# Performance work log

Measured on AMD Instinct MI355X. Metric: run time of the kernel, lower is better.

Reference implementation:

```python
import jax, jax.numpy as jnp
import numpy as np


def _lstm_cell(x, h, c, Wih, Whh, b):
    # PyTorch LSTMCell gate order: i, f, g, o; b = b_ih + b_hh
    z = x @ Wih.T + h @ Whh.T + b
    i, f, g, o = jnp.split(z, 4, axis=-1)
    c_new = jax.nn.sigmoid(f) * c + jax.nn.sigmoid(i) * jnp.tanh(g)
    h_new = jax.nn.sigmoid(o) * jnp.tanh(c_new)
    return h_new, c_new


B, T, F, H, HOR, OUT = 16384, 96, 16, 64, 24, 16


def setup_inputs() -> dict:
    key = jax.random.key(0)
    ks = jax.random.split(key, 20)
    s = 1.0 / np.sqrt(H)

    def u(k, shape):
        return jax.random.uniform(k, shape, jnp.float32, -s, s)

    return {
        "X": jax.random.normal(ks[0], (B, T, F), jnp.float32),
        "bias": jax.random.normal(ks[1], (B, 1, OUT), jnp.float32),
        "X_mask": jnp.ones((B, T), dtype=bool),
        # encoder layer 0 (in=F) and layer 1 (in=H)
        "enc_Wih0": u(ks[2], (4 * H, F)), "enc_Whh0": u(ks[3], (4 * H, H)), "enc_b0": u(ks[4], (4 * H,)),
        "enc_Wih1": u(ks[5], (4 * H, H)), "enc_Whh1": u(ks[6], (4 * H, H)), "enc_b1": u(ks[7], (4 * H,)),
        # decoder layers (in=H)
        "dec_Wih0": u(ks[8], (4 * H, H)), "dec_Whh0": u(ks[9], (4 * H, H)), "dec_b0": u(ks[10], (4 * H,)),
        "dec_Wih1": u(ks[11], (4 * H, H)), "dec_Whh1": u(ks[12], (4 * H, H)), "dec_b1": u(ks[13], (4 * H,)),
        "reg_W1": u(ks[14], (H, H)), "reg_b1": u(ks[15], (H,)),
        "reg_W2": u(ks[16], (OUT, H)), "reg_b2": u(ks[17], (OUT,)),
    }


def reference(X, bias, X_mask,
              enc_Wih0, enc_Whh0, enc_b0, enc_Wih1, enc_Whh1, enc_b1,
              dec_Wih0, dec_Whh0, dec_b0, dec_Wih1, dec_Whh1, dec_b1,
              reg_W1, reg_b1, reg_W2, reg_b2):
    b = X.shape[0]
    z = jnp.zeros((b, H), X.dtype)

    # ---- encoder: scan over time, 2 stacked LSTMCells ----
    def enc_step(carry, x_t):
        h0, c0, h1, c1 = carry
        h0, c0 = _lstm_cell(x_t, h0, c0, enc_Wih0, enc_Whh0, enc_b0)
        h1, c1 = _lstm_cell(h0, h1, c1, enc_Wih1, enc_Whh1, enc_b1)
        return (h0, c0, h1, c1), None

    (h0, _, h1, _), _ = jax.lax.scan(enc_step, (z, z, z, z),
                                     jnp.swapaxes(X, 0, 1))  # [T,B,F]

    # ---- decoder: fresh c (zeros), h from encoder, h_t starts at top-layer h ----
    last_bias = bias[:, -1]  # [B, OUT]

    def dec_step(carry, _):
        h_t, dh0, dc0, dh1, dc1 = carry
        h_t, dc0 = _lstm_cell(h_t, dh0, dc0, dec_Wih0, dec_Whh0, dec_b0)
        dh0 = h_t
        h_t, dc1 = _lstm_cell(h_t, dh1, dc1, dec_Wih1, dec_Whh1, dec_b1)
        dh1 = h_t
        y = jax.nn.relu(h_t @ reg_W1.T + reg_b1) @ reg_W2.T + reg_b2
        y = y + last_bias  # add_last_step_val=True
        return (h_t, dh0, dc0, dh1, dc1), y

    _, ys = jax.lax.scan(dec_step, (h1, h0, z, h1, z), None, length=HOR)
    return jnp.swapaxes(ys, 0, 1)  # [B, horizon, OUT]
```

## Files before the change

kernel.cpp:

```cpp
#include <hip/hip_runtime.h>

typedef short v8s __attribute__((ext_vector_type(8)));
typedef float v4f __attribute__((ext_vector_type(4)));

__device__ __forceinline__ unsigned cvtpk(float lo, float hi) {
    unsigned r;
    asm("v_cvt_pk_bf16_f32 %0, %1, %2" : "=v"(r) : "v"(lo), "v"(hi));
    return r;
}
__device__ __forceinline__ v8s pack8(float4 f0, float4 f1) {
    union { unsigned u[4]; v8s v; } r;
    r.u[0] = cvtpk(f0.x, f0.y); r.u[1] = cvtpk(f0.z, f0.w);
    r.u[2] = cvtpk(f1.x, f1.y); r.u[3] = cvtpk(f1.z, f1.w);
    return r.v;
}
__device__ __forceinline__ float sigm(float x) {
    float e = __builtin_amdgcn_exp2f(-1.44269504f * x);
    return __builtin_amdgcn_rcpf(1.0f + e);
}
__device__ __forceinline__ float tanh_(float x) {
    float e = __builtin_amdgcn_exp2f(2.88539008f * x);
    return 1.0f - 2.0f * __builtin_amdgcn_rcpf(1.0f + e);
}
__device__ __forceinline__ v4f mfma(v8s a, v8s b, v4f c) {
    return __builtin_amdgcn_mfma_f32_16x16x32_bf16(a, b, c, 0, 0, 0);
}
__device__ __forceinline__ v8s ldwf(const float* W, int rowElems, int n, int k0) {
    const float* p = W + (size_t)n * rowElems + k0;
    union { unsigned u[4]; v8s v; } r;
    #pragma unroll
    for (int j = 0; j < 4; ++j) r.u[j] = cvtpk(p[2 * j], p[2 * j + 1]);
    return r.v;
}

__global__ __launch_bounds__(256, 2) void seq2seq(
    const float* __restrict__ X,
    const float* __restrict__ bias,
    const float* __restrict__ eWih0, const float* __restrict__ eWhh0, const float* __restrict__ eb0,
    const float* __restrict__ eWih1, const float* __restrict__ eWhh1, const float* __restrict__ eb1,
    const float* __restrict__ dWih0, const float* __restrict__ dWhh0, const float* __restrict__ db0,
    const float* __restrict__ dWih1, const float* __restrict__ dWhh1, const float* __restrict__ db1,
    const float* __restrict__ rW1, const float* __restrict__ rb1,
    const float* __restrict__ rW2, const float* __restrict__ rb2,
    float* __restrict__ out)
{
    __shared__ __align__(16) short sh0[2][2048];
    __shared__ __align__(16) short sh1[2][2048];
    __shared__ __align__(16) short sy1[2048];

    const int tid  = threadIdx.x;
    const int lane = tid & 63;
    const int w    = tid >> 6;
    const int lo   = lane & 15, hi = lane >> 4;
    const int wg   = blockIdx.x;

    for (int i = tid; i < 1024; i += 256) {
        ((int*)sh0)[1024 + i] = 0;
        ((int*)sh1)[1024 + i] = 0;
    }

    const int wsidx = (w >> 1) * 512 + (((2 * w) + (lo >> 3)) & 3) * 128 + hi * 32 + (lo & 7);

    v8s wf[4][4][2];
    float bz0[4], bz1[4];
    #pragma unroll
    for (int g = 0; g < 4; ++g) {
        const int n = (w + 4 * g) * 16 + lo;
        v8s z = {0, 0, 0, 0, 0, 0, 0, 0};
        wf[0][g][0] = (hi < 2) ? ldwf(eWih0, 16, n, (hi & 1) * 8) : z;
        wf[0][g][1] = z;
        #pragma unroll
        for (int kk = 0; kk < 2; ++kk) {
            wf[1][g][kk] = ldwf(eWhh0, 64, n, kk * 32 + hi * 8);
            wf[2][g][kk] = ldwf(eWih1, 64, n, kk * 32 + hi * 8);
            wf[3][g][kk] = ldwf(eWhh1, 64, n, kk * 32 + hi * 8);
        }
        bz0[g] = eb0[g * 64 + w * 16 + lo];
        bz1[g] = eb1[g * 64 + w * 16 + lo];
    }

    float c0[2][4] = {{0.f,0.f,0.f,0.f},{0.f,0.f,0.f,0.f}};
    float c1[2][4] = {{0.f,0.f,0.f,0.f},{0.f,0.f,0.f,0.f}};
    __syncthreads();

    const float* xb = X + (size_t)(wg * 32 + lo) * 1536 + (hi & 1) * 8;

    for (int t = 0; t < 96; ++t) {
        const int pw = t & 1, pr = pw ^ 1;
        v4f acc[4][2];
        #pragma unroll
        for (int g = 0; g < 4; ++g)
            #pragma unroll
            for (int mt = 0; mt < 2; ++mt)
                acc[g][mt] = (v4f){bz0[g], bz0[g], bz0[g], bz0[g]};
        #pragma unroll
        for (int mt = 0; mt < 2; ++mt) {
            const float* p = xb + (size_t)mt * 16 * 1536 + t * 16;
            const v8s ax = pack8(*(const float4*)p, *(const float4*)(p + 4));
            #pragma unroll
            for (int g = 0; g < 4; ++g) acc[g][mt] = mfma(ax, wf[0][g][0], acc[g][mt]);
        }
        #pragma unroll
        for (int kk = 0; kk < 2; ++kk)
            #pragma unroll
            for (int mt = 0; mt < 2; ++mt) {
                const v8s ah = *(const v8s*)&sh0[pr][(mt * 2 + kk) * 512 + lane * 8];
                #pragma unroll
                for (int g = 0; g < 4; ++g) acc[g][mt] = mfma(ah, wf[1][g][kk], acc[g][mt]);
            }
        #pragma unroll
        for (int mt = 0; mt < 2; ++mt) {
            float hh[4];
            #pragma unroll
            for (int q = 0; q < 4; ++q) {
                float cc = sigm(acc[1][mt][q]) * c0[mt][q] + sigm(acc[0][mt][q]) * tanh_(acc[2][mt][q]);
                c0[mt][q] = cc;
                hh[q] = sigm(acc[3][mt][q]) * tanh_(cc);
            }
            #pragma unroll
            for (int qp = 0; qp < 2; ++qp) {
                unsigned pk = cvtpk(hh[2 * qp], hh[2 * qp + 1]);
                short* b = &sh0[pw][wsidx + mt * 1024 + qp * 16];
                b[0] = (short)pk; b[8] = (short)(pk >> 16);
            }
        }
        __syncthreads();
        #pragma unroll
        for (int g = 0; g < 4; ++g)
            #pragma unroll
            for (int mt = 0; mt < 2; ++mt)
                acc[g][mt] = (v4f){bz1[g], bz1[g], bz1[g], bz1[g]};
        #pragma unroll
        for (int kk = 0; kk < 2; ++kk)
            #pragma unroll
            for (int mt = 0; mt < 2; ++mt) {
                const v8s ah = *(const v8s*)&sh0[pw][(mt * 2 + kk) * 512 + lane * 8];
                const v8s bh = *(const v8s*)&sh1[pr][(mt * 2 + kk) * 512 + lane * 8];
                #pragma unroll
                for (int g = 0; g < 4; ++g) {
                    acc[g][mt] = mfma(ah, wf[2][g][kk], acc[g][mt]);
                    acc[g][mt] = mfma(bh, wf[3][g][kk], acc[g][mt]);
                }
            }
        #pragma unroll
        for (int mt = 0; mt < 2; ++mt) {
            float hh[4];
            #pragma unroll
            for (int q = 0; q < 4; ++q) {
                float cc = sigm(acc[1][mt][q]) * c1[mt][q] + sigm(acc[0][mt][q]) * tanh_(acc[2][mt][q]);
                c1[mt][q] = cc;
                hh[q] = sigm(acc[3][mt][q]) * tanh_(cc);
            }
            #pragma unroll
            for (int qp = 0; qp < 2; ++qp) {
                unsigned pk = cvtpk(hh[2 * qp], hh[2 * qp + 1]);
                short* b = &sh1[pw][wsidx + mt * 1024 + qp * 16];
                b[0] = (short)pk; b[8] = (short)(pk >> 16);
            }
        }
    }
    __syncthreads();

    #pragma unroll
    for (int g = 0; g < 4; ++g) {
        const int n = (w + 4 * g) * 16 + lo;
        #pragma unroll
        for (int kk = 0; kk < 2; ++kk) {
            wf[0][g][kk] = ldwf(dWih0, 64, n, kk * 32 + hi * 8);
            wf[1][g][kk] = ldwf(dWhh0, 64, n, kk * 32 + hi * 8);
            wf[2][g][kk] = ldwf(dWih1, 64, n, kk * 32 + hi * 8);
            wf[3][g][kk] = ldwf(dWhh1, 64, n, kk * 32 + hi * 8);
        }
        bz0[g] = db0[g * 64 + w * 16 + lo];
        bz1[g] = db1[g * 64 + w * 16 + lo];
    }
    v8s w1f[2], w2f[2];
    #pragma unroll
    for (int kk = 0; kk < 2; ++kk) {
        w1f[kk] = ldwf(rW1, 64, w * 16 + lo, kk * 32 + hi * 8);
        w2f[kk] = ldwf(rW2, 64, lo, kk * 32 + hi * 8);
    }
    const float hb1 = rb1[w * 16 + lo];
    const float hb2 = rb2[lo];
    float lb[2][4];
    #pragma unroll
    for (int mt = 0; mt < 2; ++mt)
        #pragma unroll
        for (int q = 0; q < 4; ++q) {
            lb[mt][q] = bias[(size_t)(wg * 32 + mt * 16 + hi * 4 + q) * 16 + lo];
            c0[mt][q] = 0.f;
            c1[mt][q] = 0.f;
        }

    for (int s = 0; s < 24; ++s) {
        const int pw = s & 1, pr = pw ^ 1;
        v4f acc[4][2];
        #pragma unroll
        for (int g = 0; g < 4; ++g)
            #pragma unroll
            for (int mt = 0; mt < 2; ++mt)
                acc[g][mt] = (v4f){bz0[g], bz0[g], bz0[g], bz0[g]};
        #pragma unroll
        for (int kk = 0; kk < 2; ++kk)
            #pragma unroll
            for (int mt = 0; mt < 2; ++mt) {
                const v8s ah = *(const v8s*)&sh1[pr][(mt * 2 + kk) * 512 + lane * 8];
                const v8s bh = *(const v8s*)&sh0[pr][(mt * 2 + kk) * 512 + lane * 8];
                #pragma unroll
                for (int g = 0; g < 4; ++g) {
                    acc[g][mt] = mfma(ah, wf[0][g][kk], acc[g][mt]);
                    acc[g][mt] = mfma(bh, wf[1][g][kk], acc[g][mt]);
                }
            }
        #pragma unroll
        for (int mt = 0; mt < 2; ++mt) {
            float hh[4];
            #pragma unroll
            for (int q = 0; q < 4; ++q) {
                float cc = sigm(acc[1][mt][q]) * c0[mt][q] + sigm(acc[0][mt][q]) * tanh_(acc[2][mt][q]);
                c0[mt][q] = cc;
                hh[q] = sigm(acc[3][mt][q]) * tanh_(cc);
            }
            #pragma unroll
            for (int qp = 0; qp < 2; ++qp) {
                unsigned pk = cvtpk(hh[2 * qp], hh[2 * qp + 1]);
                short* b = &sh0[pw][wsidx + mt * 1024 + qp * 16];
                b[0] = (short)pk; b[8] = (short)(pk >> 16);
            }
        }
        __syncthreads();
        if (w == 0 && s > 0) {
            v4f a2[2];
            #pragma unroll
            for (int mt = 0; mt < 2; ++mt) a2[mt] = (v4f){hb2, hb2, hb2, hb2};
            #pragma unroll
            for (int kk = 0; kk < 2; ++kk)
                #pragma unroll
                for (int mt = 0; mt < 2; ++mt) {
                    const v8s a = *(const v8s*)&sy1[(mt * 2 + kk) * 512 + lane * 8];
                    a2[mt] = mfma(a, w2f[kk], a2[mt]);
                }
            #pragma unroll
            for (int mt = 0; mt < 2; ++mt)
                #pragma unroll
                for (int q = 0; q < 4; ++q) {
                    size_t row = (size_t)(wg * 32 + mt * 16 + hi * 4 + q);
                    out[row * 384 + (s - 1) * 16 + lo] = a2[mt][q] + lb[mt][q];
                }
        }
        #pragma unroll
        for (int g = 0; g < 4; ++g)
            #pragma unroll
            for (int mt = 0; mt < 2; ++mt)
                acc[g][mt] = (v4f){bz1[g], bz1[g], bz1[g], bz1[g]};
        #pragma unroll
        for (int kk = 0; kk < 2; ++kk)
            #pragma unroll
            for (int mt = 0; mt < 2; ++mt) {
                const v8s ah = *(const v8s*)&sh0[pw][(mt * 2 + kk) * 512 + lane * 8];
                const v8s bh = *(const v8s*)&sh1[pr][(mt * 2 + kk) * 512 + lane * 8];
                #pragma unroll
                for (int g = 0; g < 4; ++g) {
                    acc[g][mt] = mfma(ah, wf[2][g][kk], acc[g][mt]);
                    acc[g][mt] = mfma(bh, wf[3][g][kk], acc[g][mt]);
                }
            }
        #pragma unroll
        for (int mt = 0; mt < 2; ++mt) {
            float hh[4];
            #pragma unroll
            for (int q = 0; q < 4; ++q) {
                float cc = sigm(acc[1][mt][q]) * c1[mt][q] + sigm(acc[0][mt][q]) * tanh_(acc[2][mt][q]);
                c1[mt][q] = cc;
                hh[q] = sigm(acc[3][mt][q]) * tanh_(cc);
            }
            #pragma unroll
            for (int qp = 0; qp < 2; ++qp) {
                unsigned pk = cvtpk(hh[2 * qp], hh[2 * qp + 1]);
                short* b = &sh1[pw][wsidx + mt * 1024 + qp * 16];
                b[0] = (short)pk; b[8] = (short)(pk >> 16);
            }
        }
        __syncthreads();
        v4f ay[2];
        #pragma unroll
        for (int mt = 0; mt < 2; ++mt) ay[mt] = (v4f){hb1, hb1, hb1, hb1};
        #pragma unroll
        for (int kk = 0; kk < 2; ++kk)
            #pragma unroll
            for (int mt = 0; mt < 2; ++mt) {
                const v8s ah = *(const v8s*)&sh1[pw][(mt * 2 + kk) * 512 + lane * 8];
                ay[mt] = mfma(ah, w1f[kk], ay[mt]);
            }
        #pragma unroll
        for (int mt = 0; mt < 2; ++mt) {
            #pragma unroll
            for (int qp = 0; qp < 2; ++qp) {
                unsigned pk = cvtpk(fmaxf(ay[mt][2 * qp], 0.f), fmaxf(ay[mt][2 * qp + 1], 0.f));
                short* b = &sy1[wsidx + mt * 1024 + qp * 16];
                b[0] = (short)pk; b[8] = (short)(pk >> 16);
            }
        }
    }
    __syncthreads();
    if (w == 0) {
        v4f a2[2];
        #pragma unroll
        for (int mt = 0; mt < 2; ++mt) a2[mt] = (v4f){hb2, hb2, hb2, hb2};
        #pragma unroll
        for (int kk = 0; kk < 2; ++kk)
            #pragma unroll
            for (int mt = 0; mt < 2; ++mt) {
                const v8s a = *(const v8s*)&sy1[(mt * 2 + kk) * 512 + lane * 8];
                a2[mt] = mfma(a, w2f[kk], a2[mt]);
            }
        #pragma unroll
        for (int mt = 0; mt < 2; ++mt)
            #pragma unroll
            for (int q = 0; q < 4; ++q) {
                size_t row = (size_t)(wg * 32 + mt * 16 + hi * 4 + q);
                out[row * 384 + 23 * 16 + lo] = a2[mt][q] + lb[mt][q];
            }
    }
}

extern "C" void kernel_launch(void* const* d_in, const int* in_sizes, int n_in,
                              void* d_out, int out_size, void* d_ws, size_t ws_size,
                              hipStream_t stream) {
    seq2seq<<<dim3(512), dim3(256), 0, stream>>>(
        (const float*)d_in[0],
        (const float*)d_in[1],
        (const float*)d_in[3],  (const float*)d_in[4],  (const float*)d_in[5],
        (const float*)d_in[6],  (const float*)d_in[7],  (const float*)d_in[8],
        (const float*)d_in[9],  (const float*)d_in[10], (const float*)d_in[11],
        (const float*)d_in[12], (const float*)d_in[13], (const float*)d_in[14],
        (const float*)d_in[15], (const float*)d_in[16],
        (const float*)d_in[17], (const float*)d_in[18],
        (float*)d_out);
}
```

Before: 590.5 us.

## Fuse LSTM gate nonlinearities into one cell function with fewer reciprocals; prefetch X loads

Replaces the separate sigmoid/tanh calls with an algebraically combined cell update. It uses five exp2 and two rcp per element instead of five exp2 and five rcp, which cuts transcendental-unit pressure on the recurrent critical path. It also hoists the X global loads to the top of each encoder step, reorders the recurrent MFMAs ahead of the input MFMAs so load latency is hidden, and unrolls both time loops by two. The combined formula clamps the exponent of c but not the gate exponents, so overflow to inf for large pre-activations could produce NaN. Unrolling may also raise register pressure under launch_bounds(256,2).

```diff
diff --git a/kernel.cpp b/kernel.cpp
--- a/kernel.cpp
+++ b/kernel.cpp
@@ -14,14 +14,6 @@
     r.u[2] = cvtpk(f1.x, f1.y); r.u[3] = cvtpk(f1.z, f1.w);
     return r.v;
 }
-__device__ __forceinline__ float sigm(float x) {
-    float e = __builtin_amdgcn_exp2f(-1.44269504f * x);
-    return __builtin_amdgcn_rcpf(1.0f + e);
-}
-__device__ __forceinline__ float tanh_(float x) {
-    float e = __builtin_amdgcn_exp2f(2.88539008f * x);
-    return 1.0f - 2.0f * __builtin_amdgcn_rcpf(1.0f + e);
-}
 __device__ __forceinline__ v4f mfma(v8s a, v8s b, v4f c) {
     return __builtin_amdgcn_mfma_f32_16x16x32_bf16(a, b, c, 0, 0, 0);
 }
@@ -31,6 +23,20 @@
     #pragma unroll
     for (int j = 0; j < 4; ++j) r.u[j] = cvtpk(p[2 * j], p[2 * j + 1]);
     return r.v;
+}
+
+__device__ __forceinline__ float cell(float zi, float zf, float zg, float zo, float& c) {
+    const float NL = -1.44269504f, PG = 2.88539008f;
+    float ei = __builtin_amdgcn_exp2f(NL * zi);
+    float ef = __builtin_amdgcn_exp2f(NL * zf);
+    float eg = __builtin_amdgcn_exp2f(PG * zg);
+    float Df = 1.f + ef;
+    float Dig = (1.f + ei) * (1.f + eg);
+    float cc = (c * Dig + Df * (eg - 1.f)) * __builtin_amdgcn_rcpf(Df * Dig);
+    c = cc;
+    float eo = __builtin_amdgcn_exp2f(NL * zo);
+    float ec = __builtin_amdgcn_exp2f(fminf(PG * cc, 60.f));
+    return (ec - 1.f) * __builtin_amdgcn_rcpf((1.f + eo) * (1.f + ec));
 }
 
 __global__ __launch_bounds__(256, 2) void seq2seq(
@@ -85,8 +91,16 @@
 
     const float* xb = X + (size_t)(wg * 32 + lo) * 1536 + (hi & 1) * 8;
 
+    #pragma unroll 2
     for (int t = 0; t < 96; ++t) {
         const int pw = t & 1, pr = pw ^ 1;
+        float4 xv[2][2];
+        #pragma unroll
+        for (int mt = 0; mt < 2; ++mt) {
+            const float* p = xb + (size_t)mt * 16 * 1536 + t * 16;
+            xv[mt][0] = *(const float4*)p;
+            xv[mt][1] = *(const float4*)(p + 4);
+        }
         v4f acc[4][2];
         #pragma unroll
         for (int g = 0; g < 4; ++g)
@@ -94,29 +108,25 @@
             for (int mt = 0; mt < 2; ++mt)
                 acc[g][mt] = (v4f){bz0[g], bz0[g], bz0[g], bz0[g]};
         #pragma unroll
-        for (int mt = 0; mt < 2; ++mt) {
-            const float* p = xb + (size_t)mt * 16 * 1536 + t * 16;
-            const v8s ax = pack8(*(const float4*)p, *(const float4*)(p + 4));
+        for (int kk = 0; kk < 2; ++kk)
+            #pragma unroll
+            for (int mt = 0; mt < 2; ++mt) {
+                const v8s ah = *(const v8s*)&sh0[pr][(mt * 2 + kk) * 512 + lane * 8];
+                #pragma unroll
+                for (int g = 0; g < 4; ++g) acc[g][mt] = mfma(ah, wf[1][g][kk], acc[g][mt]);
+            }
+        #pragma unroll
+        for (int mt = 0; mt < 2; ++mt) {
+            const v8s ax = pack8(xv[mt][0], xv[mt][1]);
             #pragma unroll
             for (int g = 0; g < 4; ++g) acc[g][mt] = mfma(ax, wf[0][g][0], acc[g][mt]);
         }
         #pragma unroll
-        for (int kk = 0; kk < 2; ++kk)
-            #pragma unroll
-            for (int mt = 0; mt < 2; ++mt) {
-                const v8s ah = *(const v8s*)&sh0[pr][(mt * 2 + kk) * 512 + lane * 8];
-                #pragma unroll
-                for (int g = 0; g < 4; ++g) acc[g][mt] = mfma(ah, wf[1][g][kk], acc[g][mt]);
-            }
-        #pragma unroll
         for (int mt = 0; mt < 2; ++mt) {
             float hh[4];
             #pragma unroll
-            for (int q = 0; q < 4; ++q) {
-                float cc = sigm(acc[1][mt][q]) * c0[mt][q] + sigm(acc[0][mt][q]) * tanh_(acc[2][mt][q]);
-                c0[mt][q] = cc;
-                hh[q] = sigm(acc[3][mt][q]) * tanh_(cc);
-            }
+            for (int q = 0; q < 4; ++q)
+                hh[q] = cell(acc[0][mt][q], acc[1][mt][q], acc[2][mt][q], acc[3][mt][q], c0[mt][q]);
             #pragma unroll
             for (int qp = 0; qp < 2; ++qp) {
                 unsigned pk = cvtpk(hh[2 * qp], hh[2 * qp + 1]);
@@ -146,11 +156,8 @@
         for (int mt = 0; mt < 2; ++mt) {
             float hh[4];
             #pragma unroll
-            for (int q = 0; q < 4; ++q) {
-                float cc = sigm(acc[1][mt][q]) * c1[mt][q] + sigm(acc[0][mt][q]) * tanh_(acc[2][mt][q]);
-                c1[mt][q] = cc;
-                hh[q] = sigm(acc[3][mt][q]) * tanh_(cc);
-            }
+            for (int q = 0; q < 4; ++q)
+                hh[q] = cell(acc[0][mt][q], acc[1][mt][q], acc[2][mt][q], acc[3][mt][q], c1[mt][q]);
             #pragma unroll
             for (int qp = 0; qp < 2; ++qp) {
                 unsigned pk = cvtpk(hh[2 * qp], hh[2 * qp + 1]);
@@ -192,6 +199,7 @@
             c1[mt][q] = 0.f;
         }
 
+    #pragma unroll 2
     for (int s = 0; s < 24; ++s) {
         const int pw = s & 1, pr = pw ^ 1;
         v4f acc[4][2];
@@ -216,11 +224,8 @@
         for (int mt = 0; mt < 2; ++mt) {
             float hh[4];
             #pragma unroll
-            for (int q = 0; q < 4; ++q) {
-                float cc = sigm(acc[1][mt][q]) * c0[mt][q] + sigm(acc[0][mt][q]) * tanh_(acc[2][mt][q]);
-                c0[mt][q] = cc;
-                hh[q] = sigm(acc[3][mt][q]) * tanh_(cc);
-            }
+            for (int q = 0; q < 4; ++q)
+                hh[q] = cell(acc[0][mt][q], acc[1][mt][q], acc[2][mt][q], acc[3][mt][q], c0[mt][q]);
             #pragma unroll
             for (int qp = 0; qp < 2; ++qp) {
                 unsigned pk = cvtpk(hh[2 * qp], hh[2 * qp + 1]);
@@ -269,11 +274,8 @@
         for (int mt = 0; mt < 2; ++mt) {
             float hh[4];
             #pragma unroll
-            for (int q = 0; q < 4; ++q) {
-                float cc = sigm(acc[1][mt][q]) * c1[mt][q] + sigm(acc[0][mt][q]) * tanh_(acc[2][mt][q]);
-                c1[mt][q] = cc;
-                hh[q] = sigm(acc[3][mt][q]) * tanh_(cc);
-            }
+            for (int q = 0; q < 4; ++q)
+                hh[q] = cell(acc[0][mt][q], acc[1][mt][q], acc[2][mt][q], acc[3][mt][q], c1[mt][q]);
             #pragma unroll
             for (int qp = 0; qp < 2; ++qp) {
                 unsigned pk = cvtpk(hh[2 * qp], hh[2 * qp + 1]);
```

New measurement: 575.0 us. 2.6% less time.
